# Optimization experiments

Hardware: AMD Instinct MI355X
Metric: run time of the kernel (lower is better)

## Reference

```python
import jax, jax.numpy as jnp
import numpy as np

EMBED = 1024
HEADS = 16
HEAD_DIM = EMBED // HEADS
N, SEQ = 8, 1024


def setup_inputs() -> dict:
    key = jax.random.key(0)
    ks = jax.random.split(key, 9)
    values = jax.random.normal(ks[0], (N, SEQ, EMBED), dtype=jnp.float32)
    keys_ = jax.random.normal(ks[1], (N, SEQ, EMBED), dtype=jnp.float32)
    query = jax.random.normal(ks[2], (N, SEQ, EMBED), dtype=jnp.float32)
    mask = jax.random.randint(ks[3], (N, 1, SEQ, SEQ), 0, 2, dtype=jnp.int32)
    s = 1.0 / np.sqrt(HEAD_DIM)
    Wv = jax.random.normal(ks[4], (HEAD_DIM, HEAD_DIM), dtype=jnp.float32) * s
    Wk = jax.random.normal(ks[5], (HEAD_DIM, HEAD_DIM), dtype=jnp.float32) * s
    Wq = jax.random.normal(ks[6], (HEAD_DIM, HEAD_DIM), dtype=jnp.float32) * s
    Wo = jax.random.normal(ks[7], (EMBED, EMBED), dtype=jnp.float32) * (1.0 / np.sqrt(EMBED))
    bo = jax.random.normal(ks[8], (EMBED,), dtype=jnp.float32) * 0.01
    return {"values": values, "keys": keys_, "query": query, "mask": mask,
            "Wv": Wv, "Wk": Wk, "Wq": Wq, "Wo": Wo, "bo": bo}


def reference(values, keys, query, mask, Wv, Wk, Wq, Wo, bo):
    n, q_len = query.shape[0], query.shape[1]
    v_len, k_len = values.shape[1], keys.shape[1]
    # reshape to (N, len, H, Dh); per-head linear projections share a (Dh,Dh) weight.
    v = values.reshape(n, v_len, HEADS, HEAD_DIM)
    k = keys.reshape(n, k_len, HEADS, HEAD_DIM)
    q = query.reshape(n, q_len, HEADS, HEAD_DIM)
    # torch Linear: x @ W.T
    v = jnp.einsum('nlhd,ed->nlhe', v, Wv)
    k = jnp.einsum('nlhd,ed->nlhe', k, Wk)
    q = jnp.einsum('nlhd,ed->nlhe', q, Wq)
    # scores (N,H,Q,K); mask BEFORE scaling, exactly as the torch module does
    att = jnp.einsum('nqhd,nkhd->nhqk', q, k)
    att = jnp.where(mask == 0, jnp.float32(-1e20), att)
    att = jax.nn.softmax(att / jnp.sqrt(jnp.float32(EMBED)), axis=3)
    out = jnp.einsum('nhql,nlhd->nqhd', att, v).reshape(n, q_len, EMBED)
    return out @ Wo.T + bo
```

## Files before the change

kernel.cpp:

```cpp
#include <hip/hip_runtime.h>
#include <hip/hip_bf16.h>

using bf16x8 = __attribute__((ext_vector_type(8))) __bf16;
using f32x4  = __attribute__((ext_vector_type(4))) float;

#define NB 8
#define SEQ 1024
#define HEADS 16
#define HD 64
#define EMB 1024

#if __has_builtin(__builtin_amdgcn_exp2f)
  #define EXPD(x) __builtin_amdgcn_exp2f(x)
  #define QSCALE  0.04508422f
#else
  #define EXPD(x) __expf(x)
  #define QSCALE  0.03125f
#endif

__device__ __forceinline__ int cvtpk_bf16(float lo, float hi) {
    int r;
    asm("v_cvt_pk_bf16_f32 %0, %1, %2" : "=v"(r) : "v"(lo), "v"(hi));
    return r;
}

__device__ __forceinline__ float sel0(float e, unsigned long long m) {
    float r;
    asm("v_cndmask_b32 %0, 0, %1, %2" : "=v"(r) : "v"(e), "s"(m));
    return r;
}

__device__ __forceinline__ void gld16(const __bf16* g, __bf16* l) {
    __builtin_amdgcn_global_load_lds((const __attribute__((address_space(1))) void*)g,
                                     (__attribute__((address_space(3))) void*)l, 16, 0, 0);
}

__global__ __launch_bounds__(256) void mask_perm(const int* __restrict__ mask,
                                                 unsigned long long* __restrict__ mq)
{
    __shared__ __align__(16) int Ms[128 * 68];
    const int t = threadIdx.x, w = t >> 6, lane = t & 63, quad = lane >> 4, lq = lane & 15;
    const int n = blockIdx.y;
    const int qg = blockIdx.x >> 4, kc = blockIdx.x & 15;
    const int* src = mask + ((size_t)n * SEQ + qg * 128) * SEQ + kc * 64;
    #pragma unroll
    for (int i = 0; i < 8; ++i) {
        const int c = t + i * 256, row = c >> 4, seg = c & 15;
        uint4 v = *(const uint4*)&src[(size_t)row * SEQ + seg * 4];
        *(uint4*)&Ms[row * 68 + seg * 4] = v;
    }
    __syncthreads();
    #pragma unroll
    for (int g = 0; g < 2; ++g) {
        const int row = (g * 64 + w * 16 + lq) * 68 + quad * 4;
        unsigned long long* dst = mq + ((size_t)(((n * 8 + qg) * 4 + w) * 2 + g) * 16 + kc) * 16;
        #pragma unroll
        for (int kt = 0; kt < 4; ++kt)
            #pragma unroll
            for (int r = 0; r < 4; ++r) {
                unsigned long long b = __ballot(Ms[row + kt * 16 + r] != 0);
                if (lane == 0) dst[kt * 4 + r] = b;
            }
    }
}

__global__ __launch_bounds__(256, 4) void proj_mfma(
    const float* __restrict__ q_in, const float* __restrict__ k_in, const float* __restrict__ v_in,
    const float* __restrict__ Wq, const float* __restrict__ Wk, const float* __restrict__ Wv,
    __bf16* __restrict__ qp, __bf16* __restrict__ kp, __bf16* __restrict__ vpt)
{
    const int z = blockIdx.z;
    const float* X  = (z == 0) ? q_in : (z == 1) ? k_in : v_in;
    const float* Wf = (z == 0) ? Wq   : (z == 1) ? Wk   : Wv;

    __shared__ __align__(16) __bf16 Wb[64 * 72];
    __shared__ __align__(16) __bf16 Xb[64 * 72];
    const int t = threadIdx.x;
    const int nh = blockIdx.y, n = nh >> 4, h = nh & 15;
    const int l0 = blockIdx.x * 64;
    for (int i = t; i < 4096; i += 256)
        Wb[(i >> 6) * 72 + (i & 63)] = (__bf16)Wf[i];
    {
        const int row = t >> 2, seg = (t & 3) * 16;
        const float* src = X + ((size_t)(n * SEQ + l0 + row)) * EMB + h * 64 + seg;
        union { __bf16 b[16]; uint4 u[2]; } tmp;
        #pragma unroll
        for (int jj = 0; jj < 4; ++jj) {
            float4 f = ((const float4*)src)[jj];
            tmp.b[jj*4+0] = (__bf16)f.x; tmp.b[jj*4+1] = (__bf16)f.y;
            tmp.b[jj*4+2] = (__bf16)f.z; tmp.b[jj*4+3] = (__bf16)f.w;
        }
        *(uint4*)&Xb[row * 72 + seg]     = tmp.u[0];
        *(uint4*)&Xb[row * 72 + seg + 8] = tmp.u[1];
    }
    __syncthreads();
    const int w = t >> 6, lane = t & 63, quad = lane >> 4, lr = lane & 15;
    bf16x8 af[2];
    #pragma unroll
    for (int ks = 0; ks < 2; ++ks)
        af[ks] = *(const bf16x8*)&Xb[(w * 16 + lr) * 72 + ks * 32 + quad * 8];
    const f32x4 zero4 = {0.f, 0.f, 0.f, 0.f};
    f32x4 acc[4];
    #pragma unroll
    for (int et = 0; et < 4; ++et) {
        acc[et] = zero4;
        #pragma unroll
        for (int ks = 0; ks < 2; ++ks) {
            bf16x8 bfrag = *(const bf16x8*)&Wb[(et * 16 + lr) * 72 + ks * 32 + quad * 8];
            acc[et] = __builtin_amdgcn_mfma_f32_16x16x32_bf16(af[ks], bfrag, acc[et], 0, 0, 0);
        }
    }
    if (z == 0) {
        #pragma unroll
        for (int et = 0; et < 4; ++et) acc[et] *= QSCALE;
    }
    __syncthreads();
    if (z < 2) {
        #pragma unroll
        for (int et = 0; et < 4; ++et)
            #pragma unroll
            for (int rr = 0; rr < 4; ++rr)
                Xb[(w * 16 + quad * 4 + rr) * 72 + et * 16 + lr] = (__bf16)acc[et][rr];
        __syncthreads();
        const int row = t >> 2, seg = (t & 3) * 16;
        uint4 a = *(uint4*)&Xb[row * 72 + seg];
        uint4 b = *(uint4*)&Xb[row * 72 + seg + 8];
        __bf16* outp = (z == 0) ? qp : kp;
        __bf16* dst = outp + (size_t)nh * 65536 + (size_t)(l0 + row) * 64 + seg;
        *(uint4*)&dst[0] = a;
        *(uint4*)&dst[8] = b;
    } else {
        #pragma unroll
        for (int et = 0; et < 4; ++et)
            #pragma unroll
            for (int rr = 0; rr < 4; ++rr)
                Xb[(et * 16 + lr) * 72 + w * 16 + quad * 4 + rr] = (__bf16)acc[et][rr];
        __syncthreads();
        const int e = t >> 2, seg = (t & 3) * 16;
        uint4 a = *(uint4*)&Xb[e * 72 + seg];
        uint4 b = *(uint4*)&Xb[e * 72 + seg + 8];
        __bf16* dst = vpt + (size_t)nh * 65536 + (size_t)e * SEQ + l0 + seg;
        *(uint4*)&dst[0] = a;
        *(uint4*)&dst[8] = b;
    }
}

__global__ __launch_bounds__(256, 4) void attn_mfma(
    const __bf16* __restrict__ qp, const __bf16* __restrict__ kp, const __bf16* __restrict__ vpt,
    const unsigned long long* __restrict__ mq, __bf16* __restrict__ attn_out)
{
    __shared__ __align__(16) __bf16 KV[2][2][64 * 64];
    const int t = threadIdx.x, w = t >> 6, lane = t & 63, quad = lane >> 4, lr = lane & 15;
    const int bid = blockIdx.x;
    const int nh = bid & 127, qg = bid >> 7;
    const int n = nh >> 4, h = nh & 15;
    const int q0 = qg * 128;
    const __bf16* Q  = qp  + (size_t)nh * 65536;
    const __bf16* K  = kp  + (size_t)nh * 65536;
    const __bf16* VT = vpt + (size_t)nh * 65536;

    const int wu = __builtin_amdgcn_readfirstlane(w);
    const unsigned long long* mq_w = mq + (size_t)((n * 8 + qg) * 4 + wu) * 512;

    int qrow[2];
    bf16x8 qf[2][2];
    #pragma unroll
    for (int g = 0; g < 2; ++g) {
        qrow[g] = q0 + g * 64 + w * 16 + lr;
        qf[g][0] = *(const bf16x8*)&Q[(size_t)qrow[g] * 64 + quad * 8];
        qf[g][1] = *(const bf16x8*)&Q[(size_t)qrow[g] * 64 + 32 + quad * 8];
    }

    bf16x8 onesf;
    #pragma unroll
    for (int i = 0; i < 8; ++i) onesf[i] = (__bf16)1.0f;

    const int srow = t >> 3, sc8 = t & 7;
    const int sswz = (sc8 ^ (srow & 7)) * 8;
    const int kofs = srow * 64 + sswz;
    const int vofs = srow * SEQ + sswz;

    auto issueK = [&](int kc) {
        __bf16* kb = (__bf16*)&KV[kc & 1][0][0];
        const __bf16* ksrc = K + (size_t)kc * 4096 + kofs;
        gld16(ksrc,           kb + t * 8);
        gld16(ksrc + 32 * 64, kb + t * 8 + 2048);
    };
    auto issueV = [&](int kc) {
        __bf16* vb = (__bf16*)&KV[kc & 1][1][0];
        const __bf16* vsrc = VT + (size_t)kc * 64 + vofs;
        gld16(vsrc,            vb + t * 8);
        gld16(vsrc + 32 * SEQ, vb + t * 8 + 2048);
    };

    const int s0 = ((quad ^ (lr & 7))) * 8;
    const int s1 = s0 ^ 32;

    const f32x4 zero4 = {0.f, 0.f, 0.f, 0.f};
    f32x4 O[2][4];
    f32x4 Lacc[2];
    #pragma unroll
    for (int g = 0; g < 2; ++g) {
        Lacc[g] = zero4;
        #pragma unroll
        for (int mt = 0; mt < 4; ++mt) O[g][mt] = zero4;
    }

    issueK(0); issueV(0); issueK(1);
    for (int kc = 0; kc < 16; ++kc) {
        if (kc < 15) asm volatile("s_waitcnt vmcnt(4)" ::: "memory");
        else         asm volatile("s_waitcnt vmcnt(2)" ::: "memory");
        __builtin_amdgcn_s_barrier();
        const __bf16* Kb = (const __bf16*)&KV[kc & 1][0][0];
        const __bf16* Vb = (const __bf16*)&KV[kc & 1][1][0];

        f32x4 S[2][4];
        __builtin_amdgcn_s_setprio(1);
        #pragma unroll
        for (int kt = 0; kt < 4; ++kt) {
            bf16x8 kf0 = *(const bf16x8*)&Kb[(kt * 16 + lr) * 64 + s0];
            bf16x8 kf1 = *(const bf16x8*)&Kb[(kt * 16 + lr) * 64 + s1];
            S[0][kt] = __builtin_amdgcn_mfma_f32_16x16x32_bf16(kf0, qf[0][0], zero4, 0, 0, 0);
            S[1][kt] = __builtin_amdgcn_mfma_f32_16x16x32_bf16(kf0, qf[1][0], zero4, 0, 0, 0);
            S[0][kt] = __builtin_amdgcn_mfma_f32_16x16x32_bf16(kf1, qf[0][1], S[0][kt], 0, 0, 0);
            S[1][kt] = __builtin_amdgcn_mfma_f32_16x16x32_bf16(kf1, qf[1][1], S[1][kt], 0, 0, 0);
        }
        __builtin_amdgcn_s_setprio(0);

        if (kc < 15) asm volatile("s_waitcnt vmcnt(2)" ::: "memory");
        else         asm volatile("s_waitcnt vmcnt(0)" ::: "memory");
        __builtin_amdgcn_s_barrier();
        if (kc + 1 < 16) issueV(kc + 1);

        bf16x8 pf[2][2];
        #pragma unroll
        for (int g = 0; g < 2; ++g) {
            const unsigned long long* Mg = mq_w + g * 256 + kc * 16;
            float ev[16];
            #pragma unroll
            for (int kt = 0; kt < 4; ++kt)
                #pragma unroll
                for (int r = 0; r < 4; ++r)
                    ev[kt * 4 + r] = sel0(EXPD(S[g][kt][r]), Mg[kt * 4 + r]);
            #pragma unroll
            for (int ks = 0; ks < 2; ++ks) {
                const int ka = (2 * ks) * 4, kb2 = (2 * ks + 1) * 4;
                int d0 = cvtpk_bf16(ev[ka + 0], ev[ka + 1]);
                int d1 = cvtpk_bf16(ev[ka + 2], ev[ka + 3]);
                int d2 = cvtpk_bf16(ev[kb2 + 0], ev[kb2 + 1]);
                int d3 = cvtpk_bf16(ev[kb2 + 2], ev[kb2 + 3]);
                asm("v_permlane32_swap_b32 %0, %1" : "+v"(d0), "+v"(d2));
                asm("v_permlane16_swap_b32 %0, %1" : "+v"(d0), "+v"(d2));
                asm("v_permlane32_swap_b32 %0, %1" : "+v"(d1), "+v"(d3));
                asm("v_permlane16_swap_b32 %0, %1" : "+v"(d1), "+v"(d3));
                union { int di[4]; bf16x8 v; } pb;
                pb.di[0] = d0; pb.di[1] = d1; pb.di[2] = d2; pb.di[3] = d3;
                pf[g][ks] = pb.v;
            }
        }

        __builtin_amdgcn_s_setprio(1);
        #pragma unroll
        for (int ks = 0; ks < 2; ++ks) {
            const int sv = ks ? s1 : s0;
            Lacc[0] = __builtin_amdgcn_mfma_f32_16x16x32_bf16(onesf, pf[0][ks], Lacc[0], 0, 0, 0);
            Lacc[1] = __builtin_amdgcn_mfma_f32_16x16x32_bf16(onesf, pf[1][ks], Lacc[1], 0, 0, 0);
            #pragma unroll
            for (int mt = 0; mt < 4; ++mt) {
                bf16x8 vf = *(const bf16x8*)&Vb[(mt * 16 + lr) * 64 + sv];
                O[0][mt] = __builtin_amdgcn_mfma_f32_16x16x32_bf16(vf, pf[0][ks], O[0][mt], 0, 0, 0);
                O[1][mt] = __builtin_amdgcn_mfma_f32_16x16x32_bf16(vf, pf[1][ks], O[1][mt], 0, 0, 0);
            }
        }
        __builtin_amdgcn_s_setprio(0);
        if (kc + 2 < 16) issueK(kc + 2);
    }
    #pragma unroll
    for (int g = 0; g < 2; ++g) {
        const float linv = 1.0f / Lacc[g][0];
        #pragma unroll
        for (int mt = 0; mt < 4; ++mt) {
            union { __bf16 b[4]; uint2 u; } pk;
            #pragma unroll
            for (int r = 0; r < 4; ++r) pk.b[r] = (__bf16)(O[g][mt][r] * linv);
            *(uint2*)&attn_out[((size_t)n * SEQ + qrow[g]) * EMB + h * 64 + mt * 16 + quad * 4] = pk.u;
        }
    }
}

__global__ __launch_bounds__(256) void cvt_wo(const float* __restrict__ Wo, __bf16* __restrict__ Wob)
{
    int i = blockIdx.x * 256 + threadIdx.x;
    float4 f = *(const float4*)&Wo[(size_t)i * 4];
    union { __bf16 b[4]; uint2 u; } tmp;
    tmp.b[0] = (__bf16)f.x; tmp.b[1] = (__bf16)f.y; tmp.b[2] = (__bf16)f.z; tmp.b[3] = (__bf16)f.w;
    *(uint2*)&Wob[(size_t)i * 4] = tmp.u;
}

__global__ __launch_bounds__(256, 3) void out_gemm_mfma(
    const __bf16* __restrict__ A, const __bf16* __restrict__ B,
    const float* __restrict__ bo, float* __restrict__ out)
{
    __shared__ __align__(16) __bf16 AB[2][(64 + 128) * 64];
    const int t = threadIdx.x, w = t >> 6, lane = t & 63, quad = lane >> 4, lr = lane & 15;
    const int wr = (w >> 1) * 32, wc = (w & 1) * 64;
    const int r0 = blockIdx.y * 64, e0 = blockIdx.x * 128;

    const int srow = t >> 3, sj = t & 7;
    const int sswz = (sj ^ (srow & 7)) * 8;

    auto issue = [&](int st) {
        __bf16* buf = (__bf16*)&AB[st & 1][0];
        const __bf16* as = A + (size_t)(r0 + srow) * EMB + st * 64 + sswz;
        const __bf16* bs = B + (size_t)(e0 + srow) * EMB + st * 64 + sswz;
        gld16(as,            buf + t * 8);
        gld16(as + 32 * EMB, buf + t * 8 + 2048);
        gld16(bs,            buf + 4096 + t * 8);
        gld16(bs + 32 * EMB, buf + 4096 + t * 8 + 2048);
        gld16(bs + 64 * EMB, buf + 4096 + t * 8 + 4096);
        gld16(bs + 96 * EMB, buf + 4096 + t * 8 + 6144);
    };

    const int s0 = (quad ^ (lr & 7)) * 8, s1 = s0 ^ 32;
    const f32x4 zero4 = {0.f, 0.f, 0.f, 0.f};
    f32x4 acc[2][4];
    #pragma unroll
    for (int mt = 0; mt < 2; ++mt)
        #pragma unroll
        for (int nt = 0; nt < 4; ++nt) acc[mt][nt] = zero4;

    issue(0);
    for (int st = 0; st < 16; ++st) {
        __syncthreads();
        if (st + 1 < 16) issue(st + 1);
        const __bf16* buf = (const __bf16*)&AB[st & 1][0];
        #pragma unroll
        for (int ks = 0; ks < 2; ++ks) {
            const int sv = ks ? s1 : s0;
            bf16x8 af[2], bf[4];
            #pragma unroll
            for (int mt = 0; mt < 2; ++mt)
                af[mt] = *(const bf16x8*)&buf[(wr + mt * 16 + lr) * 64 + sv];
            #pragma unroll
            for (int nt = 0; nt < 4; ++nt)
                bf[nt] = *(const bf16x8*)&buf[4096 + (wc + nt * 16 + lr) * 64 + sv];
            __builtin_amdgcn_s_setprio(1);
            #pragma unroll
            for (int mt = 0; mt < 2; ++mt)
                #pragma unroll
                for (int nt = 0; nt < 4; ++nt)
                    acc[mt][nt] = __builtin_amdgcn_mfma_f32_16x16x32_bf16(af[mt], bf[nt], acc[mt][nt], 0, 0, 0);
            __builtin_amdgcn_s_setprio(0);
        }
    }
    float bv[4];
    #pragma unroll
    for (int nt = 0; nt < 4; ++nt) bv[nt] = bo[e0 + wc + nt * 16 + lr];
    #pragma unroll
    for (int mt = 0; mt < 2; ++mt)
        #pragma unroll
        for (int nt = 0; nt < 4; ++nt)
            #pragma unroll
            for (int rr = 0; rr < 4; ++rr)
                out[(size_t)(r0 + wr + mt * 16 + quad * 4 + rr) * EMB + e0 + wc + nt * 16 + lr] =
                    acc[mt][nt][rr] + bv[nt];
}

extern "C" void kernel_launch(void* const* d_in, const int* in_sizes, int n_in,
                              void* d_out, int out_size, void* d_ws, size_t ws_size,
                              hipStream_t stream) {
    const float* values = (const float*)d_in[0];
    const float* keys   = (const float*)d_in[1];
    const float* query  = (const float*)d_in[2];
    const int*   mask   = (const int*)d_in[3];
    const float* Wv     = (const float*)d_in[4];
    const float* Wk     = (const float*)d_in[5];
    const float* Wq     = (const float*)d_in[6];
    const float* Wo     = (const float*)d_in[7];
    const float* bo     = (const float*)d_in[8];
    float* out = (float*)d_out;

    const size_t per = (size_t)NB * HEADS * SEQ * HD;
    __bf16* qp   = (__bf16*)d_ws;
    __bf16* kp   = qp + per;
    __bf16* vpt  = kp + per;
    __bf16* attn = vpt + per;
    __bf16* Wob  = attn + (size_t)NB * SEQ * EMB;
    unsigned long long* maskq = (unsigned long long*)(Wob + (size_t)EMB * EMB);

    mask_perm<<<dim3(128, NB), 256, 0, stream>>>(mask, maskq);
    proj_mfma<<<dim3(16, 128, 3), 256, 0, stream>>>(query, keys, values, Wq, Wk, Wv, qp, kp, vpt);
    cvt_wo<<<1024, 256, 0, stream>>>(Wo, Wob);
    attn_mfma<<<1024, 256, 0, stream>>>(qp, kp, vpt, maskq, attn);
    out_gemm_mfma<<<dim3(EMB / 128, NB * SEQ / 64), 256, 0, stream>>>(attn, Wob, bo, out);
}
```

Before: 255.5 us.

## Fold Wo conversion into mask kernel; loop projection over four row tiles with prefetch

The standalone Wo fp32-to-bf16 conversion kernel is removed and its work is done by an extra row of blocks in the mask permutation kernel, saving one launch. The projection kernel now processes four 64-row tiles per block, converting the per-head weight once per block instead of once per 64 rows. It also prefetches the next tile's inputs into registers while the current tile's MFMAs run. The cost is a quarter as many projection blocks (1536), which may reduce latency hiding, plus extra barriers per tile.

Result: no change. 260.1 us (+1.8%).

```diff
diff --git a/kernel.cpp b/kernel.cpp
--- a/kernel.cpp
+++ b/kernel.cpp
@@ -36,10 +36,26 @@
 }
 
 __global__ __launch_bounds__(256) void mask_perm(const int* __restrict__ mask,
-                                                 unsigned long long* __restrict__ mq)
+                                                 unsigned long long* __restrict__ mq,
+                                                 const float* __restrict__ Wo,
+                                                 __bf16* __restrict__ Wob)
 {
     __shared__ __align__(16) int Ms[128 * 68];
-    const int t = threadIdx.x, w = t >> 6, lane = t & 63, quad = lane >> 4, lq = lane & 15;
+    const int t = threadIdx.x;
+    if (blockIdx.y == NB) {
+        const size_t base = (size_t)blockIdx.x * 8192;
+        #pragma unroll
+        for (int jj = 0; jj < 8; ++jj) {
+            const size_t off = base + (size_t)jj * 1024 + (size_t)t * 4;
+            float4 f = *(const float4*)&Wo[off];
+            union { __bf16 b[4]; uint2 u; } tmp;
+            tmp.b[0] = (__bf16)f.x; tmp.b[1] = (__bf16)f.y;
+            tmp.b[2] = (__bf16)f.z; tmp.b[3] = (__bf16)f.w;
+            *(uint2*)&Wob[off] = tmp.u;
+        }
+        return;
+    }
+    const int w = t >> 6, lane = t & 63, quad = lane >> 4, lq = lane & 15;
     const int n = blockIdx.y;
     const int qg = blockIdx.x >> 4, kc = blockIdx.x & 15;
     const int* src = mask + ((size_t)n * SEQ + qg * 128) * SEQ + kc * 64;
@@ -77,71 +93,84 @@
     __shared__ __align__(16) __bf16 Xb[64 * 72];
     const int t = threadIdx.x;
     const int nh = blockIdx.y, n = nh >> 4, h = nh & 15;
-    const int l0 = blockIdx.x * 64;
+    const int l0 = blockIdx.x * 256;
     for (int i = t; i < 4096; i += 256)
         Wb[(i >> 6) * 72 + (i & 63)] = (__bf16)Wf[i];
-    {
-        const int row = t >> 2, seg = (t & 3) * 16;
-        const float* src = X + ((size_t)(n * SEQ + l0 + row)) * EMB + h * 64 + seg;
-        union { __bf16 b[16]; uint4 u[2]; } tmp;
-        #pragma unroll
-        for (int jj = 0; jj < 4; ++jj) {
-            float4 f = ((const float4*)src)[jj];
-            tmp.b[jj*4+0] = (__bf16)f.x; tmp.b[jj*4+1] = (__bf16)f.y;
-            tmp.b[jj*4+2] = (__bf16)f.z; tmp.b[jj*4+3] = (__bf16)f.w;
-        }
-        *(uint4*)&Xb[row * 72 + seg]     = tmp.u[0];
-        *(uint4*)&Xb[row * 72 + seg + 8] = tmp.u[1];
-    }
-    __syncthreads();
+
+    const int row = t >> 2, seg = (t & 3) * 16;
+    const float* src0 = X + ((size_t)(n * SEQ + l0 + row)) * EMB + h * 64 + seg;
+
+    float4 xr[4];
+    #pragma unroll
+    for (int jj = 0; jj < 4; ++jj) xr[jj] = ((const float4*)src0)[jj];
+
     const int w = t >> 6, lane = t & 63, quad = lane >> 4, lr = lane & 15;
-    bf16x8 af[2];
-    #pragma unroll
-    for (int ks = 0; ks < 2; ++ks)
-        af[ks] = *(const bf16x8*)&Xb[(w * 16 + lr) * 72 + ks * 32 + quad * 8];
     const f32x4 zero4 = {0.f, 0.f, 0.f, 0.f};
-    f32x4 acc[4];
-    #pragma unroll
-    for (int et = 0; et < 4; ++et) {
-        acc[et] = zero4;
-        #pragma unroll
-        for (int ks = 0; ks < 2; ++ks) {
-            bf16x8 bfrag = *(const bf16x8*)&Wb[(et * 16 + lr) * 72 + ks * 32 + quad * 8];
-            acc[et] = __builtin_amdgcn_mfma_f32_16x16x32_bf16(af[ks], bfrag, acc[et], 0, 0, 0);
-        }
-    }
-    if (z == 0) {
-        #pragma unroll
-        for (int et = 0; et < 4; ++et) acc[et] *= QSCALE;
-    }
-    __syncthreads();
-    if (z < 2) {
-        #pragma unroll
-        for (int et = 0; et < 4; ++et)
-            #pragma unroll
-            for (int rr = 0; rr < 4; ++rr)
-                Xb[(w * 16 + quad * 4 + rr) * 72 + et * 16 + lr] = (__bf16)acc[et][rr];
+
+    for (int st = 0; st < 4; ++st) {
         __syncthreads();
-        const int row = t >> 2, seg = (t & 3) * 16;
-        uint4 a = *(uint4*)&Xb[row * 72 + seg];
-        uint4 b = *(uint4*)&Xb[row * 72 + seg + 8];
-        __bf16* outp = (z == 0) ? qp : kp;
-        __bf16* dst = outp + (size_t)nh * 65536 + (size_t)(l0 + row) * 64 + seg;
-        *(uint4*)&dst[0] = a;
-        *(uint4*)&dst[8] = b;
-    } else {
-        #pragma unroll
-        for (int et = 0; et < 4; ++et)
-            #pragma unroll
-            for (int rr = 0; rr < 4; ++rr)
-                Xb[(et * 16 + lr) * 72 + w * 16 + quad * 4 + rr] = (__bf16)acc[et][rr];
+        {
+            union { __bf16 b[16]; uint4 u[2]; } tmp;
+            #pragma unroll
+            for (int jj = 0; jj < 4; ++jj) {
+                float4 f = xr[jj];
+                tmp.b[jj*4+0] = (__bf16)f.x; tmp.b[jj*4+1] = (__bf16)f.y;
+                tmp.b[jj*4+2] = (__bf16)f.z; tmp.b[jj*4+3] = (__bf16)f.w;
+            }
+            *(uint4*)&Xb[row * 72 + seg]     = tmp.u[0];
+            *(uint4*)&Xb[row * 72 + seg + 8] = tmp.u[1];
+        }
         __syncthreads();
-        const int e = t >> 2, seg = (t & 3) * 16;
-        uint4 a = *(uint4*)&Xb[e * 72 + seg];
-        uint4 b = *(uint4*)&Xb[e * 72 + seg + 8];
-        __bf16* dst = vpt + (size_t)nh * 65536 + (size_t)e * SEQ + l0 + seg;
-        *(uint4*)&dst[0] = a;
-        *(uint4*)&dst[8] = b;
+        bf16x8 af[2];
+        #pragma unroll
+        for (int ks = 0; ks < 2; ++ks)
+            af[ks] = *(const bf16x8*)&Xb[(w * 16 + lr) * 72 + ks * 32 + quad * 8];
+        if (st < 3) {
+            const float* srcn = src0 + (size_t)(st + 1) * 64 * EMB;
+            #pragma unroll
+            for (int jj = 0; jj < 4; ++jj) xr[jj] = ((const float4*)srcn)[jj];
+        }
+        f32x4 acc[4];
+        #pragma unroll
+        for (int et = 0; et < 4; ++et) {
+            acc[et] = zero4;
+            #pragma unroll
+            for (int ks = 0; ks < 2; ++ks) {
+                bf16x8 bfrag = *(const bf16x8*)&Wb[(et * 16 + lr) * 72 + ks * 32 + quad * 8];
+                acc[et] = __builtin_amdgcn_mfma_f32_16x16x32_bf16(af[ks], bfrag, acc[et], 0, 0, 0);
+            }
+        }
+        if (z == 0) {
+            #pragma unroll
+            for (int et = 0; et < 4; ++et) acc[et] *= QSCALE;
+        }
+        __syncthreads();
+        if (z < 2) {
+            #pragma unroll
+            for (int et = 0; et < 4; ++et)
+                #pragma unroll
+                for (int rr = 0; rr < 4; ++rr)
+                    Xb[(w * 16 + quad * 4 + rr) * 72 + et * 16 + lr] = (__bf16)acc[et][rr];
+            __syncthreads();
+            uint4 a = *(uint4*)&Xb[row * 72 + seg];
+            uint4 b = *(uint4*)&Xb[row * 72 + seg + 8];
+            __bf16* outp = (z == 0) ? qp : kp;
+            __bf16* dst = outp + (size_t)nh * 65536 + (size_t)(l0 + st * 64 + row) * 64 + seg;
+            *(uint4*)&dst[0] = a;
+            *(uint4*)&dst[8] = b;
+        } else {
+            #pragma unroll
+            for (int et = 0; et < 4; ++et)
+                #pragma unroll
+                for (int rr = 0; rr < 4; ++rr)
+                    Xb[(et * 16 + lr) * 72 + w * 16 + quad * 4 + rr] = (__bf16)acc[et][rr];
+            __syncthreads();
+            uint4 a = *(uint4*)&Xb[row * 72 + seg];
+            uint4 b = *(uint4*)&Xb[row * 72 + seg + 8];
+            __bf16* dst = vpt + (size_t)nh * 65536 + (size_t)row * SEQ + (l0 + st * 64) + seg;
+            *(uint4*)&dst[0] = a;
+            *(uint4*)&dst[8] = b;
+        }
     }
 }
 
@@ -288,15 +317,6 @@
     }
 }
 
-__global__ __launch_bounds__(256) void cvt_wo(const float* __restrict__ Wo, __bf16* __restrict__ Wob)
-{
-    int i = blockIdx.x * 256 + threadIdx.x;
-    float4 f = *(const float4*)&Wo[(size_t)i * 4];
-    union { __bf16 b[4]; uint2 u; } tmp;
-    tmp.b[0] = (__bf16)f.x; tmp.b[1] = (__bf16)f.y; tmp.b[2] = (__bf16)f.z; tmp.b[3] = (__bf16)f.w;
-    *(uint2*)&Wob[(size_t)i * 4] = tmp.u;
-}
-
 __global__ __launch_bounds__(256, 3) void out_gemm_mfma(
     const __bf16* __restrict__ A, const __bf16* __restrict__ B,
     const float* __restrict__ bo, float* __restrict__ out)
@@ -388,9 +408,8 @@
     __bf16* Wob  = attn + (size_t)NB * SEQ * EMB;
     unsigned long long* maskq = (unsigned long long*)(Wob + (size_t)EMB * EMB);
 
-    mask_perm<<<dim3(128, NB), 256, 0, stream>>>(mask, maskq);
-    proj_mfma<<<dim3(16, 128, 3), 256, 0, stream>>>(query, keys, values, Wq, Wk, Wv, qp, kp, vpt);
-    cvt_wo<<<1024, 256, 0, stream>>>(Wo, Wob);
+    mask_perm<<<dim3(128, NB + 1), 256, 0, stream>>>(mask, maskq, Wo, Wob);
+    proj_mfma<<<dim3(4, 128, 3), 256, 0, stream>>>(query, keys, values, Wq, Wk, Wv, qp, kp, vpt);
     attn_mfma<<<1024, 256, 0, stream>>>(qp, kp, vpt, maskq, attn);
     out_gemm_mfma<<<dim3(EMB / 128, NB * SEQ / 64), 256, 0, stream>>>(attn, Wob, bo, out);
 }
```
